# Optimization experiments

Measured on AMD Instinct MI355X. Metric: run time of the kernel, lower is better.

Reference implementation:

```python
import jax, jax.numpy as jnp
import numpy as np

B, T, C = 2, 2048, 1024
NUM_HEADS, NUM_KV_HEADS, HEAD_DIM = 16, 8, 64
R = NUM_HEADS // NUM_KV_HEADS  # q heads per kv head
WINDOW = 512
HIDDEN = 4096
SOFT_CAP = 50.0


def setup_inputs() -> dict:
    key = jax.random.key(0)
    ks = jax.random.split(key, 10)
    std = 0.02
    return {
        "x": jax.random.normal(ks[0], (B, T, C), jnp.float32),
        "kurtosis_sum": jnp.zeros((), jnp.float32),
        "rms1_scale": jnp.zeros((C,), jnp.float32),
        "q_kernel": std * jax.random.normal(ks[1], (C, R, NUM_KV_HEADS, HEAD_DIM), jnp.float32),
        "k_kernel": std * jax.random.normal(ks[2], (C, NUM_KV_HEADS, HEAD_DIM), jnp.float32),
        "v_kernel": std * jax.random.normal(ks[3], (C, NUM_KV_HEADS, HEAD_DIM), jnp.float32),
        "out_kernel": std * jax.random.normal(ks[4], (R, NUM_KV_HEADS, HEAD_DIM, C), jnp.float32),
        "rms2_scale": jnp.zeros((C,), jnp.float32),
        "gate_kernel": std * jax.random.normal(ks[5], (C, HIDDEN), jnp.float32),
        "up_kernel": std * jax.random.normal(ks[6], (C, HIDDEN), jnp.float32),
        "down_kernel": std * jax.random.normal(ks[7], (HIDDEN, C), jnp.float32),
    }


def sine_table(features, length, max_timescale=1e6):
    fraction = jnp.arange(0, features, 2, dtype=jnp.float32) / features
    rot_freq = 1.0 / (max_timescale ** fraction)
    sinusoid = jnp.arange(length, dtype=jnp.float32)[:, None] * rot_freq[None, :]
    sinusoid = jnp.concatenate([sinusoid, sinusoid], axis=-1)  # (T, features)
    return jnp.sin(sinusoid), jnp.cos(sinusoid)


def rotate_half(x):
    x1, x2 = jnp.split(x, 2, axis=-1)
    return jnp.concatenate([-x2, x1], axis=-1)


def rms_norm(x, scale):
    var = jnp.mean(jnp.square(x.astype(jnp.float32)), axis=-1, keepdims=True)
    normed = (x * jax.lax.rsqrt(var + 1e-6)).astype(x.dtype)
    return normed * (1 + scale)


def excess_kurtosis(emb):
    mean = jnp.mean(emb, axis=-1, keepdims=True)
    std = jnp.std(emb, axis=-1, keepdims=True)
    centralized = emb - mean
    fourth = jnp.mean(centralized ** 4, axis=-1, keepdims=True)
    kurt = jnp.squeeze(fourth / (std ** 4 + 1e-6), axis=-1).reshape(-1) - 3
    return jnp.sum(jnp.maximum(kurt, 0.0))


def reference(x, kurtosis_sum, rms1_scale, q_kernel, k_kernel, v_kernel,
              out_kernel, rms2_scale, gate_kernel, up_kernel, down_kernel):
    Bc, Tc, Cc = x.shape
    # sliding-window causal mask: j <= i and |i - j| < WINDOW
    idx = jnp.arange(Tc)
    causal = idx[:, None] >= idx[None, :]
    band = jnp.abs(idx[:, None] - idx[None, :]) < WINDOW
    mask = (causal & band)[None, None, None]  # (1,1,1,T,T) for brhsd scores

    # --- attention ---
    attn_in = rms_norm(x, rms1_scale)
    q = jnp.einsum('bsm,mrhk->brhsk', attn_in, q_kernel)
    k = jnp.einsum('bdm,mhk->bhdk', attn_in, k_kernel)
    v = jnp.einsum('bdm,mhv->bhdv', attn_in, v_kernel)

    sin, cos = sine_table(HEAD_DIM, Tc, max_timescale=1e6)
    q = q * cos[None, None, None] + rotate_half(q) * sin[None, None, None]
    k = k * cos[None, None] + rotate_half(k) * sin[None, None]

    scale = jax.lax.rsqrt(jnp.asarray(HEAD_DIM, dtype=x.dtype))
    qk = jnp.einsum('brhsk,bhdk->brhsd', q, k) * scale
    qk = jnp.tanh(qk / SOFT_CAP) * SOFT_CAP
    probs = jax.nn.softmax(qk.astype(jnp.float32), where=mask).astype(x.dtype)
    qkv = jnp.einsum('brhsd,bhdv->brhsv', probs, v)
    attn_out = jnp.einsum('brhsv,rhvm->bsm', qkv, out_kernel)
    x = x + attn_out

    # --- SwiGLU MLP ---
    mlp_in = rms_norm(x, rms2_scale)
    gate = jax.nn.silu(mlp_in @ gate_kernel)
    up = mlp_in @ up_kernel
    x = x + (up * gate) @ down_kernel

    return (x, kurtosis_sum + excess_kurtosis(x))
```

## Files before the change

### kernel.cpp

```cpp
#include <hip/hip_runtime.h>
#include <hip/hip_bf16.h>

typedef __attribute__((ext_vector_type(8))) short short8;
typedef __attribute__((ext_vector_type(4))) float f32x4;
typedef __attribute__((ext_vector_type(4))) int int4v;
typedef __attribute__((ext_vector_type(8))) int int8v;

#define DEVFN static __device__ __forceinline__

DEVFN float bf2f(unsigned short u) {
    unsigned int i = ((unsigned int)u) << 16;
    float f; __builtin_memcpy(&f, &i, 4); return f;
}
DEVFN unsigned short f2bf(float f) {
    unsigned int i; __builtin_memcpy(&i, &f, 4);
    unsigned int r = i + 0x7fffu + ((i >> 16) & 1u);
    return (unsigned short)(r >> 16);
}
DEVFN unsigned char f2fp8(float f) {
    int r = __builtin_amdgcn_cvt_pk_fp8_f32(f, f, 0, false);
    return (unsigned char)(r & 0xff);
}
DEVFN float fastrcp(float x) { return __builtin_amdgcn_rcpf(x); }

DEVFN void load_lds16(const void* g, void* l) {
    __builtin_amdgcn_global_load_lds(
        (__attribute__((address_space(1))) void*)g,
        (__attribute__((address_space(3))) void*)l, 16, 0, 0);
}

DEVFN f32x4 mfma_fp8(int8v a, int8v b, f32x4 c) {
    return __builtin_amdgcn_mfma_scale_f32_16x16x128_f8f6f4(
        a, b, c, 0, 0, 0, 0x7F7F7F7F, 0, 0x7F7F7F7F);
}

constexpr int Bsz = 2, T = 2048, C = 1024;
constexpr int NH = 16, NKV = 8, HD = 64;
constexpr int HID = 4096;
constexpr int NTOK = Bsz * T;
constexpr size_t MiB = 1024 * 1024;

constexpr size_t OFF_WQKV = 0;
constexpr size_t OFF_WOUT = 4 * MiB;
constexpr size_t OFF_WGATE = 6 * MiB;
constexpr size_t OFF_WUP = 10 * MiB;
constexpr size_t OFF_WDOWN = 14 * MiB;
constexpr size_t OFF_XN1 = 18 * MiB;
constexpr size_t OFF_QKVP = 26 * MiB;
constexpr size_t OFF_P2 = 26 * MiB;
constexpr size_t OFF_QB = 58 * MiB;
constexpr size_t OFF_KB = 66 * MiB;
constexpr size_t OFF_VT = 70 * MiB;
constexpr size_t OFF_CTX = 74 * MiB;
constexpr size_t OFF_X2 = 82 * MiB;
constexpr size_t OFF_XN2 = 98 * MiB;
constexpr size_t OFF_G = 102 * MiB;
constexpr size_t OFF_P4 = 118 * MiB;

__global__ __launch_bounds__(256) void prep_kernel(
    const float* __restrict__ qk, const float* __restrict__ kk2,
    const float* __restrict__ vk, const float* __restrict__ ok,
    const float* __restrict__ gk, const float* __restrict__ uk,
    const float* __restrict__ dk,
    unsigned short* __restrict__ wqkv, unsigned short* __restrict__ wout,
    unsigned char* __restrict__ wgate, unsigned char* __restrict__ wup,
    unsigned char* __restrict__ wdown,
    const float* __restrict__ x, const float* __restrict__ rms1_scale,
    unsigned short* __restrict__ xn1) {
    __shared__ float t[32][33];
    __shared__ float red[4];
    int id = blockIdx.x;
    int tid = threadIdx.x;
    if (id >= 15360) {
        int row = id - 15360;
        const float4 v = *(const float4*)&x[(size_t)row * 1024 + tid * 4];
        float ss = v.x * v.x + v.y * v.y + v.z * v.z + v.w * v.w;
#pragma unroll
        for (int m = 32; m; m >>= 1) ss += __shfl_xor(ss, m, 64);
        if ((tid & 63) == 0) red[tid >> 6] = ss;
        __syncthreads();
        float tot = red[0] + red[1] + red[2] + red[3];
        float inv = rsqrtf(tot * (1.f / 1024.f) + 1e-6f);
        const float4 sc = *(const float4*)&rms1_scale[tid * 4];
        size_t o = (size_t)row * 1024 + tid * 4;
        xn1[o + 0] = f2bf(v.x * inv * (1.f + sc.x));
        xn1[o + 1] = f2bf(v.y * inv * (1.f + sc.y));
        xn1[o + 2] = f2bf(v.z * inv * (1.f + sc.z));
        xn1[o + 3] = f2bf(v.w * inv * (1.f + sc.w));
        return;
    }
    const float* in; int K, N, nx, base; int fp8 = 0;
    unsigned short* out16 = nullptr; unsigned char* out8 = nullptr;
    if (id < 1024)       { in = qk;  out16 = wqkv;                       K = 1024; N = 1024; nx = 32;  base = 0; }
    else if (id < 1536)  { in = kk2; out16 = wqkv + (size_t)1024 * 1024; K = 1024; N = 512;  nx = 16;  base = 1024; }
    else if (id < 2048)  { in = vk;  out16 = wqkv + (size_t)1536 * 1024; K = 1024; N = 512;  nx = 16;  base = 1536; }
    else if (id < 3072)  { in = ok;  out16 = wout;                       K = 1024; N = 1024; nx = 32;  base = 2048; }
    else if (id < 7168)  { in = gk;  out8 = wgate; fp8 = 1;              K = 1024; N = 4096; nx = 128; base = 3072; }
    else if (id < 11264) { in = uk;  out8 = wup; fp8 = 1;                K = 1024; N = 4096; nx = 128; base = 7168; }
    else                 { in = dk;  out8 = wdown; fp8 = 1;              K = 4096; N = 1024; nx = 32;  base = 11264; }
    int lid = id - base;
    int n0 = (lid % nx) * 32, k0 = (lid / nx) * 32;
    int tx = tid & 31, ty = tid >> 5;
#pragma unroll
    for (int i = 0; i < 4; i++)
        t[ty + 8 * i][tx] = in[(size_t)(k0 + ty + 8 * i) * N + n0 + tx];
    __syncthreads();
    if (fp8) {
#pragma unroll
        for (int i = 0; i < 4; i++)
            out8[(size_t)(n0 + ty + 8 * i) * K + k0 + tx] = f2fp8(t[tx][ty + 8 * i] * 16.f);
    } else {
#pragma unroll
        for (int i = 0; i < 4; i++)
            out16[(size_t)(n0 + ty + 8 * i) * K + k0 + tx] = f2bf(t[tx][ty + 8 * i]);
    }
}

__global__ __launch_bounds__(256) void gemm128(const unsigned short* __restrict__ A,
                                               const unsigned short* __restrict__ Bt,
                                               unsigned short* __restrict__ Cp,
                                               int N, int K, int lda, int ldb,
                                               size_t zA, size_t zB, size_t zC) {
    __shared__ __align__(16) unsigned short As[128 * 32];
    __shared__ __align__(16) unsigned short Bs[128 * 32];
    A += (size_t)blockIdx.z * zA;
    Bt += (size_t)blockIdx.z * zB;
    const int tid = threadIdx.x;
    const int lane = tid & 63, w = tid >> 6;
    const int quad = lane >> 4, l15 = lane & 15;
    const int wr = w >> 1, wc = w & 1;
    const int m0 = blockIdx.y * 128, n0 = blockIdx.x * 128;

    f32x4 acc[4][4];
#pragma unroll
    for (int i = 0; i < 4; i++)
#pragma unroll
        for (int j = 0; j < 4; j++) acc[i][j] = f32x4{0.f, 0.f, 0.f, 0.f};

    const int stRow = (w << 4) + (lane >> 2);
    const int stCol = (lane & 3) << 3;

    for (int kk = 0; kk < K; kk += 32) {
#pragma unroll
        for (int i = 0; i < 2; i++) {
            load_lds16(A + (size_t)(m0 + (i << 6) + stRow) * lda + kk + stCol,
                       &As[((i << 6) + (w << 4)) * 32]);
            load_lds16(Bt + (size_t)(n0 + (i << 6) + stRow) * ldb + kk + stCol,
                       &Bs[((i << 6) + (w << 4)) * 32]);
        }
        __syncthreads();
        short8 a[4], b[4];
#pragma unroll
        for (int mi = 0; mi < 4; mi++)
            a[mi] = *(const short8*)&As[(wr * 64 + mi * 16 + l15) * 32 + quad * 8];
#pragma unroll
        for (int ni = 0; ni < 4; ni++)
            b[ni] = *(const short8*)&Bs[(wc * 64 + ni * 16 + l15) * 32 + quad * 8];
#pragma unroll
        for (int mi = 0; mi < 4; mi++)
#pragma unroll
            for (int ni = 0; ni < 4; ni++)
                acc[mi][ni] = __builtin_amdgcn_mfma_f32_16x16x32_bf16(a[mi], b[ni], acc[mi][ni], 0, 0, 0);
        __syncthreads();
    }
#pragma unroll
    for (int mi = 0; mi < 4; mi++)
#pragma unroll
        for (int ni = 0; ni < 4; ni++)
#pragma unroll
            for (int r = 0; r < 4; r++) {
                int row = m0 + wr * 64 + mi * 16 + quad * 4 + r;
                int col = n0 + wc * 64 + ni * 16 + l15;
                Cp[(size_t)blockIdx.z * zC + (size_t)row * N + col] = f2bf(acc[mi][ni][r]);
            }
}

DEVFN int8v read_frag8(const unsigned char* buf, int rb, int quad) {
    int base = rb * 128;
    int h0 = (2 * quad) ^ (rb & 7);
    int h1 = (2 * quad + 1) ^ (rb & 7);
    int4v lo = *(const int4v*)&buf[base + h0 * 16];
    int4v hi = *(const int4v*)&buf[base + h1 * 16];
    return int8v{lo.x, lo.y, lo.z, lo.w, hi.x, hi.y, hi.z, hi.w};
}

__global__ __launch_bounds__(256) void gateup_kernel(const unsigned char* __restrict__ A,
                                                     const unsigned char* __restrict__ Bg,
                                                     const unsigned char* __restrict__ Bu,
                                                     unsigned char* __restrict__ out) {
    __shared__ __align__(16) unsigned char As[128 * 128];
    __shared__ __align__(16) unsigned char Gs[64 * 128];
    __shared__ __align__(16) unsigned char Us[64 * 128];
    const int tid = threadIdx.x;
    const int lane = tid & 63, w = tid >> 6;
    const int quad = lane >> 4, l15 = lane & 15;
    const int wr = w >> 1, wc = w & 1;
    const int m0 = blockIdx.y * 128, n0 = blockIdx.x * 64;

    f32x4 aG[4][2], aU[4][2];
#pragma unroll
    for (int i = 0; i < 4; i++)
#pragma unroll
        for (int j = 0; j < 2; j++) { aG[i][j] = f32x4{0.f, 0.f, 0.f, 0.f}; aU[i][j] = f32x4{0.f, 0.f, 0.f, 0.f}; }

    const int lrow = lane >> 3;
    const int hA = (lane & 7) ^ lrow;

    for (int kk = 0; kk < 1024; kk += 128) {
#pragma unroll
        for (int j = 0; j < 4; j++) {
            int i = w * 4 + j;
            int r = i * 8 + lrow;
            load_lds16(A + (size_t)(m0 + r) * 1024 + kk + hA * 16, &As[i * 1024]);
        }
#pragma unroll
        for (int j = 0; j < 2; j++) {
            int i = w * 2 + j;
            int r = i * 8 + lrow;
            load_lds16(Bg + (size_t)(n0 + r) * 1024 + kk + hA * 16, &Gs[i * 1024]);
            load_lds16(Bu + (size_t)(n0 + r) * 1024 + kk + hA * 16, &Us[i * 1024]);
        }
        __syncthreads();
        int8v a[4], bg[2], bu[2];
#pragma unroll
        for (int mi = 0; mi < 4; mi++)
            a[mi] = read_frag8(As, wr * 64 + mi * 16 + l15, quad);
#pragma unroll
        for (int ni = 0; ni < 2; ni++) {
            bg[ni] = read_frag8(Gs, wc * 32 + ni * 16 + l15, quad);
            bu[ni] = read_frag8(Us, wc * 32 + ni * 16 + l15, quad);
        }
#pragma unroll
        for (int mi = 0; mi < 4; mi++)
#pragma unroll
            for (int ni = 0; ni < 2; ni++) {
                aG[mi][ni] = mfma_fp8(a[mi], bg[ni], aG[mi][ni]);
                aU[mi][ni] = mfma_fp8(a[mi], bu[ni], aU[mi][ni]);
            }
        __syncthreads();
    }
#pragma unroll
    for (int mi = 0; mi < 4; mi++)
#pragma unroll
        for (int ni = 0; ni < 2; ni++)
#pragma unroll
            for (int r = 0; r < 4; r++) {
                int row = m0 + wr * 64 + mi * 16 + quad * 4 + r;
                int col = n0 + wc * 32 + ni * 16 + l15;
                float vg = aG[mi][ni][r] * (1.f / 64.f);
                float vu = aU[mi][ni][r] * (1.f / 64.f);
                float s = vg * fastrcp(1.f + __expf(-vg));
                out[(size_t)row * 4096 + col] = f2fp8(s * vu * 8.f);
            }
}

__global__ __launch_bounds__(256) void down_gemm(const unsigned char* __restrict__ A,
                                                 const unsigned char* __restrict__ Bt,
                                                 unsigned short* __restrict__ Cp) {
    __shared__ __align__(16) unsigned char As[128 * 128];
    __shared__ __align__(16) unsigned char Bs[128 * 128];
    const int tid = threadIdx.x;
    const int lane = tid & 63, w = tid >> 6;
    const int quad = lane >> 4, l15 = lane & 15;
    const int wr = w >> 1, wc = w & 1;
    const int m0 = blockIdx.y * 128, n0 = blockIdx.x * 128;
    const int kbase = blockIdx.z * 1024;

    f32x4 acc[4][4];
#pragma unroll
    for (int i = 0; i < 4; i++)
#pragma unroll
        for (int j = 0; j < 4; j++) acc[i][j] = f32x4{0.f, 0.f, 0.f, 0.f};

    const int lrow = lane >> 3;
    const int hA = (lane & 7) ^ lrow;

    for (int kk = 0; kk < 1024; kk += 128) {
#pragma unroll
        for (int j = 0; j < 4; j++) {
            int i = w * 4 + j;
            int r = i * 8 + lrow;
            load_lds16(A + (size_t)(m0 + r) * 4096 + kbase + kk + hA * 16, &As[i * 1024]);
            load_lds16(Bt + (size_t)(n0 + r) * 4096 + kbase + kk + hA * 16, &Bs[i * 1024]);
        }
        __syncthreads();
        int8v a[4], b[4];
#pragma unroll
        for (int mi = 0; mi < 4; mi++)
            a[mi] = read_frag8(As, wr * 64 + mi * 16 + l15, quad);
#pragma unroll
        for (int ni = 0; ni < 4; ni++)
            b[ni] = read_frag8(Bs, wc * 64 + ni * 16 + l15, quad);
#pragma unroll
        for (int mi = 0; mi < 4; mi++)
#pragma unroll
            for (int ni = 0; ni < 4; ni++)
                acc[mi][ni] = mfma_fp8(a[mi], b[ni], acc[mi][ni]);
        __syncthreads();
    }
    const size_t Z = (size_t)NTOK * 1024;
#pragma unroll
    for (int mi = 0; mi < 4; mi++)
#pragma unroll
        for (int ni = 0; ni < 4; ni++)
#pragma unroll
            for (int r = 0; r < 4; r++) {
                int row = m0 + wr * 64 + mi * 16 + quad * 4 + r;
                int col = n0 + wc * 64 + ni * 16 + l15;
                Cp[(size_t)blockIdx.z * Z + (size_t)row * 1024 + col] =
                    f2bf(acc[mi][ni][r] * (1.f / 128.f));
            }
}

__global__ __launch_bounds__(256) void reduce_out(const unsigned short* __restrict__ p,
                                                  const float* __restrict__ x,
                                                  const float* __restrict__ scale,
                                                  float* __restrict__ x2,
                                                  unsigned char* __restrict__ xn2,
                                                  const float* __restrict__ ksum,
                                                  float* __restrict__ outk) {
    __shared__ float red[4];
    int row = blockIdx.x, tid = threadIdx.x;
    if (row == 0 && tid == 0) outk[0] = ksum[0];
    size_t base = (size_t)row * 1024 + tid * 4;
    const size_t Z = (size_t)NTOK * 1024;
    float4 v = *(const float4*)&x[base];
#pragma unroll
    for (int z = 0; z < 4; z++) {
        ushort4 u = *(const ushort4*)&p[base + z * Z];
        v.x += bf2f(u.x); v.y += bf2f(u.y); v.z += bf2f(u.z); v.w += bf2f(u.w);
    }
    *(float4*)&x2[base] = v;
    float ss = v.x * v.x + v.y * v.y + v.z * v.z + v.w * v.w;
#pragma unroll
    for (int m = 32; m; m >>= 1) ss += __shfl_xor(ss, m, 64);
    if ((tid & 63) == 0) red[tid >> 6] = ss;
    __syncthreads();
    float tot = red[0] + red[1] + red[2] + red[3];
    float inv = rsqrtf(tot * (1.f / 1024.f) + 1e-6f) * 4.f;
    const float4 sc = *(const float4*)&scale[tid * 4];
    xn2[base + 0] = f2fp8(v.x * inv * (1.f + sc.x));
    xn2[base + 1] = f2fp8(v.y * inv * (1.f + sc.y));
    xn2[base + 2] = f2fp8(v.z * inv * (1.f + sc.z));
    xn2[base + 3] = f2fp8(v.w * inv * (1.f + sc.w));
}

__global__ __launch_bounds__(256) void reduce_down(const unsigned short* __restrict__ p,
                                                   const float* __restrict__ x2,
                                                   float* __restrict__ outx,
                                                   float* __restrict__ outk) {
    __shared__ float red[4], r2[4], r4[4];
    int row = blockIdx.x, tid = threadIdx.x;
    size_t base = (size_t)row * 1024 + tid * 4;
    const size_t Z = (size_t)NTOK * 1024;
    float4 v = *(const float4*)&x2[base];
#pragma unroll
    for (int z = 0; z < 4; z++) {
        ushort4 u = *(const ushort4*)&p[base + z * Z];
        v.x += bf2f(u.x); v.y += bf2f(u.y); v.z += bf2f(u.z); v.w += bf2f(u.w);
    }
    *(float4*)&outx[base] = v;
    float s = v.x + v.y + v.z + v.w;
#pragma unroll
    for (int m = 32; m; m >>= 1) s += __shfl_xor(s, m, 64);
    if ((tid & 63) == 0) red[tid >> 6] = s;
    __syncthreads();
    float mean = (red[0] + red[1] + red[2] + red[3]) * (1.f / 1024.f);
    float cx = v.x - mean, cy = v.y - mean, cz = v.z - mean, cw = v.w - mean;
    float x2v = cx * cx, y2 = cy * cy, z2 = cz * cz, w2 = cw * cw;
    float c2 = x2v + y2 + z2 + w2;
    float c4 = x2v * x2v + y2 * y2 + z2 * z2 + w2 * w2;
#pragma unroll
    for (int m = 32; m; m >>= 1) {
        c2 += __shfl_xor(c2, m, 64);
        c4 += __shfl_xor(c4, m, 64);
    }
    if ((tid & 63) == 0) { r2[tid >> 6] = c2; r4[tid >> 6] = c4; }
    __syncthreads();
    if (tid == 0) {
        float m2 = (r2[0] + r2[1] + r2[2] + r2[3]) * (1.f / 1024.f);
        float m4 = (r4[0] + r4[1] + r4[2] + r4[3]) * (1.f / 1024.f);
        float kurt = m4 / (m2 * m2 + 1e-6f) - 3.f;
        if (kurt > 0.f) atomicAdd(outk, kurt);
    }
}

__global__ __launch_bounds__(256) void ropevt_kernel(const unsigned short* __restrict__ qkvp,
                                                     unsigned short* __restrict__ qb,
                                                     unsigned short* __restrict__ kb,
                                                     unsigned short* __restrict__ vt) {
    __shared__ float sv[32], cv[32];
    __shared__ unsigned short tile[64][68];
    const size_t Z = (size_t)NTOK * 2048;
    int id = blockIdx.x;
    int tid = threadIdx.x;
    if (id < NTOK) {
        int tok = id;
        int b = tok >> 11, t = tok & 2047;
        if (tid < 32) {
            float fr = (float)tid * (1.f / 32.f);
            float freq = powf(1e6f, -fr);
            float a = (float)t * freq;
            sv[tid] = sinf(a);
            cv[tid] = cosf(a);
        }
        __syncthreads();
        const unsigned short* r0 = qkvp + (size_t)tok * 2048;
        const unsigned short* r1 = r0 + Z;
#pragma unroll
        for (int e = tid; e < 1536; e += 256) {
            int u = e >> 6, d = e & 63;
            int col = (u < 16) ? (u * 64 + d) : (1024 + (u - 16) * 64 + d);
            int pcol = (d < 32) ? col + 32 : col - 32;
            float sgn = (d < 32) ? -1.f : 1.f;
            float vc = bf2f(r0[col]) + bf2f(r1[col]);
            float vp = bf2f(r0[pcol]) + bf2f(r1[pcol]);
            float o = vc * cv[d & 31] + sgn * vp * sv[d & 31];
            if (u < 16)
                qb[((size_t)(b * 16 + u) * 2048 + t) * 64 + d] = f2bf(o);
            else
                kb[((size_t)(b * 8 + (u - 16)) * 2048 + t) * 64 + d] = f2bf(o);
        }
    } else {
        int lid = id - NTOK;
        int b = lid >> 8, h = (lid >> 5) & 7, t0 = (lid & 31) * 64;
        int d = tid & 63, tr = tid >> 6;
#pragma unroll
        for (int i = 0; i < 16; i++) {
            int t = tr + i * 4;
            size_t gi = (size_t)(b * 2048 + t0 + t) * 2048 + 1536 + h * 64 + d;
            tile[t][d] = f2bf(bf2f(qkvp[gi]) + bf2f(qkvp[gi + Z]));
        }
        __syncthreads();
        int tt = tid & 63, dr = tid >> 6;
#pragma unroll
        for (int i = 0; i < 16; i++) {
            int dd = dr + i * 4;
            vt[((size_t)(b * 8 + h) * 64 + dd) * 2048 + t0 + tt] = tile[tt][dd];
        }
    }
}

__global__ __launch_bounds__(256) void attn_kernel(const unsigned short* __restrict__ qb,
                                                   const unsigned short* __restrict__ kb,
                                                   const unsigned short* __restrict__ vt,
                                                   unsigned short* __restrict__ ctx) {
    __shared__ __align__(16) unsigned short P[4][2][16 * 64];
    const int tid = threadIdx.x, lane = tid & 63, w = tid >> 6;
    const int quad = lane >> 4, l15 = lane & 15;
    const int qt = blockIdx.x, H = blockIdx.y, b = blockIdx.z;
    const int hkv = H & 7;
    const int qw = qt * 64 + w * 16;

    const unsigned short* qbase = qb + ((size_t)(b * 16 + H) * 2048 + qw) * 64;
    short8 aq0 = *(const short8*)(qbase + (size_t)l15 * 64 + quad * 8);
    short8 aq1 = *(const short8*)(qbase + (size_t)l15 * 64 + 32 + quad * 8);

    const unsigned short* kbase = kb + (size_t)(b * 8 + hkv) * 2048 * 64;
    const unsigned short* vbase = vt + (size_t)(b * 8 + hkv) * 64 * 2048;

    const short bf1 = (short)0x3F80;
    const short8 ones = {bf1, bf1, bf1, bf1, bf1, bf1, bf1, bf1};

    f32x4 O[4];
#pragma unroll
    for (int i = 0; i < 4; i++) O[i] = f32x4{0.f, 0.f, 0.f, 0.f};
    f32x4 lacc = f32x4{0.f, 0.f, 0.f, 0.f};

    int kstart = qw - 511;
    if (kstart < 0) kstart = 0;
    kstart &= ~63;
    int buf = 0;

    for (int k0 = kstart; k0 <= qw + 15; k0 += 64) {
        f32x4 S[4];
#pragma unroll
        for (int c = 0; c < 4; c++) {
            const unsigned short* kp = kbase + (size_t)(k0 + c * 16 + l15) * 64 + quad * 8;
            short8 kf0 = *(const short8*)kp;
            short8 kf1 = *(const short8*)(kp + 32);
            f32x4 s = __builtin_amdgcn_mfma_f32_16x16x32_bf16(aq0, kf0, f32x4{0.f, 0.f, 0.f, 0.f}, 0, 0, 0);
            s = __builtin_amdgcn_mfma_f32_16x16x32_bf16(aq1, kf1, s, 0, 0, 0);
            S[c] = s;
        }
        unsigned short* Pw = P[w][buf];
#pragma unroll
        for (int c = 0; c < 4; c++)
#pragma unroll
            for (int r = 0; r < 4; r++) {
                int i = qw + quad * 4 + r;
                int j = k0 + c * 16 + l15;
                float Sc = fminf(3200.f, fmaxf(-3200.f, S[c][r]));
                float e = __expf(Sc * 0.005f);
                float y = 50.f - 100.f * fastrcp(e + 1.f);
                bool ok = (j <= i) && ((i - j) < 512);
                float pv = ok ? __expf(y) : 0.f;
                Pw[(quad * 4 + r) * 64 + c * 16 + l15] = f2bf(pv);
            }
        asm volatile("s_waitcnt lgkmcnt(0)" ::: "memory");
        short8 pf0 = *(const short8*)&Pw[l15 * 64 + quad * 8];
        short8 pf1 = *(const short8*)&Pw[l15 * 64 + 32 + quad * 8];
#pragma unroll
        for (int ni = 0; ni < 4; ni++) {
            const unsigned short* vp = vbase + (size_t)(ni * 16 + l15) * 2048 + k0;
            short8 vf0 = *(const short8*)(vp + quad * 8);
            short8 vf1 = *(const short8*)(vp + 32 + quad * 8);
            O[ni] = __builtin_amdgcn_mfma_f32_16x16x32_bf16(pf0, vf0, O[ni], 0, 0, 0);
            O[ni] = __builtin_amdgcn_mfma_f32_16x16x32_bf16(pf1, vf1, O[ni], 0, 0, 0);
        }
        lacc = __builtin_amdgcn_mfma_f32_16x16x32_bf16(pf0, ones, lacc, 0, 0, 0);
        lacc = __builtin_amdgcn_mfma_f32_16x16x32_bf16(pf1, ones, lacc, 0, 0, 0);
        buf ^= 1;
    }
#pragma unroll
    for (int r = 0; r < 4; r++) {
        float inv = fastrcp(lacc[r]);
        int i = qw + quad * 4 + r;
        size_t tok = (size_t)b * 2048 + i;
#pragma unroll
        for (int ni = 0; ni < 4; ni++)
            ctx[tok * 1024 + H * 64 + ni * 16 + l15] = f2bf(O[ni][r] * inv);
    }
}

extern "C" void kernel_launch(void* const* d_in, const int* in_sizes, int n_in,
                              void* d_out, int out_size, void* d_ws, size_t ws_size,
                              hipStream_t stream) {
    const float* x = (const float*)d_in[0];
    const float* ksum = (const float*)d_in[1];
    const float* rms1_scale = (const float*)d_in[2];
    const float* q_w = (const float*)d_in[3];
    const float* k_w = (const float*)d_in[4];
    const float* v_w = (const float*)d_in[5];
    const float* out_w = (const float*)d_in[6];
    const float* rms2_scale = (const float*)d_in[7];
    const float* gate_w = (const float*)d_in[8];
    const float* up_w = (const float*)d_in[9];
    const float* down_w = (const float*)d_in[10];

    char* ws = (char*)d_ws;
    unsigned short* wqkv = (unsigned short*)(ws + OFF_WQKV);
    unsigned short* wout = (unsigned short*)(ws + OFF_WOUT);
    unsigned char* wgate = (unsigned char*)(ws + OFF_WGATE);
    unsigned char* wup = (unsigned char*)(ws + OFF_WUP);
    unsigned char* wdown = (unsigned char*)(ws + OFF_WDOWN);
    unsigned short* xn1 = (unsigned short*)(ws + OFF_XN1);
    unsigned short* qkvp = (unsigned short*)(ws + OFF_QKVP);
    unsigned short* p2 = (unsigned short*)(ws + OFF_P2);
    unsigned short* qb = (unsigned short*)(ws + OFF_QB);
    unsigned short* kb = (unsigned short*)(ws + OFF_KB);
    unsigned short* vtb = (unsigned short*)(ws + OFF_VT);
    unsigned short* ctx = (unsigned short*)(ws + OFF_CTX);
    float* x2 = (float*)(ws + OFF_X2);
    unsigned char* xn2 = (unsigned char*)(ws + OFF_XN2);
    unsigned char* g = (unsigned char*)(ws + OFF_G);
    unsigned short* p4 = (unsigned short*)(ws + OFF_P4);
    float* outx = (float*)d_out;
    float* outk = outx + (size_t)NTOK * C;

    prep_kernel<<<15360 + NTOK, 256, 0, stream>>>(
        q_w, k_w, v_w, out_w, gate_w, up_w, down_w,
        wqkv, wout, wgate, wup, wdown, x, rms1_scale, xn1);

    gemm128<<<dim3(2048 / 128, NTOK / 128, 2), 256, 0, stream>>>(
        xn1, wqkv, qkvp, 2048, 512, 1024, 1024, 512, 512, (size_t)NTOK * 2048);

    ropevt_kernel<<<NTOK + 512, 256, 0, stream>>>(qkvp, qb, kb, vtb);

    attn_kernel<<<dim3(T / 64, NH, Bsz), 256, 0, stream>>>(qb, kb, vtb, ctx);

    gemm128<<<dim3(1024 / 128, NTOK / 128, 4), 256, 0, stream>>>(
        ctx, wout, p2, 1024, 256, 1024, 1024, 256, 256, (size_t)NTOK * 1024);
    reduce_out<<<NTOK, 256, 0, stream>>>(p2, x, rms2_scale, x2, xn2, ksum, outk);

    gateup_kernel<<<dim3(HID / 64, NTOK / 128), 256, 0, stream>>>(xn2, wgate, wup, g);

    down_gemm<<<dim3(1024 / 128, NTOK / 128, 4), 256, 0, stream>>>(g, wdown, p4);
    reduce_down<<<NTOK, 256, 0, stream>>>(p4, x2, outx, outk);

    (void)in_sizes; (void)n_in; (void)out_size; (void)ws_size;
}
```

Before: 379.3 us.

## Stage K and V tiles in shared memory for attention kernel

```diff
diff --git a/kernel.cpp b/kernel.cpp
--- a/kernel.cpp
+++ b/kernel.cpp
@@ -445,6 +445,8 @@
                                                    const unsigned short* __restrict__ kb,
                                                    const unsigned short* __restrict__ vt,
                                                    unsigned short* __restrict__ ctx) {
+    __shared__ __align__(16) unsigned short Ks[64 * 64];
+    __shared__ __align__(16) unsigned short Vs[64 * 64];
     __shared__ __align__(16) unsigned short P[4][2][16 * 64];
     const int tid = threadIdx.x, lane = tid & 63, w = tid >> 6;
     const int quad = lane >> 4, l15 = lane & 15;
@@ -467,18 +469,32 @@
     for (int i = 0; i < 4; i++) O[i] = f32x4{0.f, 0.f, 0.f, 0.f};
     f32x4 lacc = f32x4{0.f, 0.f, 0.f, 0.f};
 
-    int kstart = qw - 511;
-    if (kstart < 0) kstart = 0;
-    kstart &= ~63;
+    const int srow = lane >> 3;
+    const int schunk = (lane & 7) ^ srow;
+    const int sw = l15 & 7;
+
+    int kstartB = qt * 64 - 511;
+    if (kstartB < 0) kstartB = 0;
+    kstartB &= ~63;
+    const int kendB = qt * 64 + 63;
     int buf = 0;
 
-    for (int k0 = kstart; k0 <= qw + 15; k0 += 64) {
+    for (int k0 = kstartB; k0 <= kendB; k0 += 64) {
+#pragma unroll
+        for (int rr = 0; rr < 2; rr++) {
+            int row = w * 8 + rr * 32 + srow;
+            load_lds16(kbase + (size_t)(k0 + row) * 64 + schunk * 8,
+                       &Ks[(w * 8 + rr * 32) * 64]);
+            load_lds16(vbase + (size_t)row * 2048 + k0 + schunk * 8,
+                       &Vs[(w * 8 + rr * 32) * 64]);
+        }
+        __syncthreads();
         f32x4 S[4];
 #pragma unroll
         for (int c = 0; c < 4; c++) {
-            const unsigned short* kp = kbase + (size_t)(k0 + c * 16 + l15) * 64 + quad * 8;
-            short8 kf0 = *(const short8*)kp;
-            short8 kf1 = *(const short8*)(kp + 32);
+            const unsigned short* kp = &Ks[(c * 16 + l15) * 64];
+            short8 kf0 = *(const short8*)&kp[(quad ^ sw) * 8];
+            short8 kf1 = *(const short8*)&kp[((4 + quad) ^ sw) * 8];
             f32x4 s = __builtin_amdgcn_mfma_f32_16x16x32_bf16(aq0, kf0, f32x4{0.f, 0.f, 0.f, 0.f}, 0, 0, 0);
             s = __builtin_amdgcn_mfma_f32_16x16x32_bf16(aq1, kf1, s, 0, 0, 0);
             S[c] = s;
@@ -502,15 +518,16 @@
         short8 pf1 = *(const short8*)&Pw[l15 * 64 + 32 + quad * 8];
 #pragma unroll
         for (int ni = 0; ni < 4; ni++) {
-            const unsigned short* vp = vbase + (size_t)(ni * 16 + l15) * 2048 + k0;
-            short8 vf0 = *(const short8*)(vp + quad * 8);
-            short8 vf1 = *(const short8*)(vp + 32 + quad * 8);
+            const unsigned short* vp = &Vs[(ni * 16 + l15) * 64];
+            short8 vf0 = *(const short8*)&vp[(quad ^ sw) * 8];
+            short8 vf1 = *(const short8*)&vp[((4 + quad) ^ sw) * 8];
             O[ni] = __builtin_amdgcn_mfma_f32_16x16x32_bf16(pf0, vf0, O[ni], 0, 0, 0);
             O[ni] = __builtin_amdgcn_mfma_f32_16x16x32_bf16(pf1, vf1, O[ni], 0, 0, 0);
         }
         lacc = __builtin_amdgcn_mfma_f32_16x16x32_bf16(pf0, ones, lacc, 0, 0, 0);
         lacc = __builtin_amdgcn_mfma_f32_16x16x32_bf16(pf1, ones, lacc, 0, 0, 0);
         buf ^= 1;
+        __syncthreads();
     }
 #pragma unroll
     for (int r = 0; r < 4; r++) {
```

New measurement: 343.3 us. 9.5% less time.
